# Performance work log

Hardware: AMD Instinct MI355X
Metric: run time of the kernel (lower is better)

## Reference

```python
import jax, jax.numpy as jnp
import numpy as np

N = 100000   # nodes
E = 1600000  # edges
D = 64       # in/hidden channels


def setup_inputs() -> dict:
    key = jax.random.key(0)
    ks = jax.random.split(key, 8)
    x = jax.random.normal(ks[0], (N, D), dtype=jnp.float32)
    edge_index = jax.random.randint(ks[1], (2, E), 0, N, dtype=jnp.int32)
    s = 1.0 / np.sqrt(D)
    W1 = jax.random.uniform(ks[2], (D, D), jnp.float32, -s, s)
    W2 = jax.random.uniform(ks[3], (D, D), jnp.float32, -s, s)
    W3 = jax.random.uniform(ks[4], (D, D), jnp.float32, -s, s)
    b1 = jnp.zeros((D,), jnp.float32)
    b2 = jnp.zeros((D,), jnp.float32)
    b3 = jnp.zeros((D,), jnp.float32)
    return {"x": x, "edge_index": edge_index,
            "W1": W1, "b1": b1, "W2": W2, "b2": b2, "W3": W3, "b3": b3}


def _gcn_conv(x, src, dst, deg_inv_sqrt, W, b):
    # norm = d^{-1/2}[src] * d^{-1/2}[dst] (symmetric GCN normalization w/ self-loops)
    norm = deg_inv_sqrt[src] * deg_inv_sqrt[dst]        # [E+N]
    h = x @ W                                           # [N, D] dense GEMM
    msg = h[src] * norm[:, None]                        # gather + scale
    out = jax.ops.segment_sum(msg, dst, num_segments=x.shape[0])  # scatter-add
    return out + b


def reference(x, edge_index, W1, b1, W2, b2, W3, b3):
    n = x.shape[0]
    loop = jnp.arange(n, dtype=edge_index.dtype)
    src = jnp.concatenate([edge_index[0], loop])        # add self-loops
    dst = jnp.concatenate([edge_index[1], loop])
    deg = jax.ops.segment_sum(jnp.ones_like(src, x.dtype), dst, num_segments=n)
    deg_inv_sqrt = jnp.where(deg > 0, jax.lax.rsqrt(jnp.maximum(deg, 1.0)), 0.0)

    h = _gcn_conv(x, src, dst, deg_inv_sqrt, W1, b1)
    h = jax.nn.relu(h)                                  # dropout is identity (eval)
    h = _gcn_conv(h, src, dst, deg_inv_sqrt, W2, b2)
    h = jax.nn.relu(h)
    out = _gcn_conv(h, src, dst, deg_inv_sqrt, W3, b3)
    return out
```

## Files before the change

### kernel.cpp

```cpp
#include <hip/hip_runtime.h>
#include <hip/hip_fp16.h>
#include <type_traits>

#define DCH 64
#define NBSHIFT 8
#define BROWS 256
#define MAXNB 512
#define CAPB 5120
#define CAP 8192
#define CHUNK 4096
#define SCT 512

__global__ __launch_bounds__(SCT) void bucket_scatter(const int* __restrict__ src,
        const int* __restrict__ dst, int* __restrict__ cursor,
        unsigned int* __restrict__ tmp, int E, int NB) {
    __shared__ int hist[MAXNB];
    __shared__ int loff[MAXNB];
    __shared__ int res[MAXNB];
    __shared__ unsigned int stage[CHUNK];
    __shared__ unsigned short stgb[CHUNK];
    const int base_e = blockIdx.x * CHUNK;
    const int nloc = min(CHUNK, E - base_e);
    const int t = threadIdx.x;
    if (t < NB) hist[t] = 0;
    __syncthreads();
    unsigned int pk[CHUNK / SCT];
    int bk[CHUNK / SCT], rk[CHUNK / SCT];
    #pragma unroll
    for (int c = 0; c < CHUNK / SCT; ++c) {
        int i = t + c * SCT;
        if (i < nloc) {
            int d = dst[base_e + i];
            int b = d >> NBSHIFT;
            rk[c] = atomicAdd(&hist[b], 1);
            bk[c] = b;
            pk[c] = ((unsigned int)(d & (BROWS - 1)) << 24) |
                    (unsigned int)src[base_e + i];
        }
    }
    __syncthreads();
    int v = (t < NB) ? hist[t] : 0;
    loff[t] = v;
    __syncthreads();
    for (int o = 1; o < MAXNB; o <<= 1) {
        int add = (t >= o) ? loff[t - o] : 0;
        __syncthreads();
        loff[t] += add;
        __syncthreads();
    }
    int excl = loff[t] - v;
    loff[t] = excl;
    if (t < NB) res[t] = v ? (t * CAPB + atomicAdd(&cursor[t], v)) : 0;
    __syncthreads();
    #pragma unroll
    for (int c = 0; c < CHUNK / SCT; ++c) {
        int i = t + c * SCT;
        if (i < nloc) {
            int p = loff[bk[c]] + rk[c];
            stage[p] = pk[c];
            stgb[p]  = (unsigned short)bk[c];
        }
    }
    __syncthreads();
    for (int i = t; i < nloc; i += SCT) {
        int b = stgb[i];
        tmp[res[b] + (i - loff[b])] = stage[i];
    }
}

__global__ __launch_bounds__(BROWS) void bucket_to_csr(
        const unsigned int* __restrict__ tmp, const int* __restrict__ cursor,
        int2* __restrict__ range, int* __restrict__ srcs,
        float* __restrict__ dinv, int N) {
    __shared__ int hist[BROWS];
    __shared__ int off[BROWS];
    __shared__ int cur[BROWS];
    __shared__ int stage[CAP];
    const int b = blockIdx.x;
    const int base = b * CAPB;
    const int count = cursor[b];
    const int t = threadIdx.x;
    hist[t] = 0;
    __syncthreads();
    for (int i = t; i < count; i += BROWS)
        atomicAdd(&hist[tmp[base + i] >> 24], 1);
    __syncthreads();
    int v = hist[t];
    off[t] = v;
    __syncthreads();
    for (int o = 1; o < BROWS; o <<= 1) {
        int add = (t >= o) ? off[t - o] : 0;
        __syncthreads();
        off[t] += add;
        __syncthreads();
    }
    int excl = off[t] - v;
    cur[t] = excl;
    int node = (b << NBSHIFT) + t;
    if (node < N) {
        range[node] = make_int2(base + excl, base + excl + v);
        dinv[node]  = rsqrtf((float)v + 1.0f);
    }
    __syncthreads();
    const bool st = (count <= CAP);
    for (int i = t; i < count; i += BROWS) {
        unsigned int p = tmp[base + i];
        int low = p >> 24;
        int s = (int)(p & 0xFFFFFFu);
        int pos = atomicAdd(&cur[low], 1);
        if (st) stage[pos] = s;
        else    srcs[base + pos] = s;
    }
    __syncthreads();
    if (st)
        for (int i = t; i < count; i += BROWS) srcs[base + i] = stage[i];
}

template<typename InT>
__global__ __launch_bounds__(256, 4) void gemm64(const InT* __restrict__ A,
        const float* __restrict__ W, const float* __restrict__ dinv,
        __half* __restrict__ H, int nrows) {
    __shared__ float Wl[64 * 64];
    __shared__ float Al[64 * 68];
    #pragma unroll
    for (int j = 0; j < 4; ++j) {
        int idx = (int)threadIdx.x + j * 256;
        float4 w = ((const float4*)W)[idx];
        *(float4*)&Wl[(idx >> 4) * 64 + (idx & 15) * 4] = w;
    }
    const int tx = threadIdx.x & 15;
    const int ty = threadIdx.x >> 4;
    const int c0 = tx * 4, r0 = ty * 4;
    const int ntiles = (nrows + 63) >> 6;
    for (int tile = blockIdx.x; tile < ntiles; tile += gridDim.x) {
        const int rowbase = tile << 6;
        const int rmax = min(64, nrows - rowbase);
        __syncthreads();
        #pragma unroll
        for (int j = 0; j < 4; ++j) {
            int idx = (int)threadIdx.x + j * 256;
            int r = idx >> 4, kq = idx & 15;
            float4 a;
            if (r < rmax) {
                if constexpr (std::is_same<InT, float>::value) {
                    a = *(const float4*)(A + (size_t)(rowbase + r) * 64 + kq * 4);
                } else {
                    unsigned long long u = *(const unsigned long long*)
                        ((const __half*)A + (size_t)(rowbase + r) * 64 + kq * 4);
                    union { unsigned long long u; __half2 h[2]; } cv; cv.u = u;
                    float2 f0 = __half22float2(cv.h[0]);
                    float2 f1 = __half22float2(cv.h[1]);
                    a = make_float4(f0.x, f0.y, f1.x, f1.y);
                }
            } else a = make_float4(0.f, 0.f, 0.f, 0.f);
            *(float4*)&Al[r * 68 + kq * 4] = a;
        }
        __syncthreads();
        float acc[4][4] = {};
        #pragma unroll 8
        for (int k = 0; k < 64; ++k) {
            float4 wv = *(const float4*)&Wl[k * 64 + c0];
            float a0 = Al[(r0 + 0) * 68 + k];
            float a1 = Al[(r0 + 1) * 68 + k];
            float a2 = Al[(r0 + 2) * 68 + k];
            float a3 = Al[(r0 + 3) * 68 + k];
            acc[0][0] += a0 * wv.x; acc[0][1] += a0 * wv.y; acc[0][2] += a0 * wv.z; acc[0][3] += a0 * wv.w;
            acc[1][0] += a1 * wv.x; acc[1][1] += a1 * wv.y; acc[1][2] += a1 * wv.z; acc[1][3] += a1 * wv.w;
            acc[2][0] += a2 * wv.x; acc[2][1] += a2 * wv.y; acc[2][2] += a2 * wv.z; acc[2][3] += a2 * wv.w;
            acc[3][0] += a3 * wv.x; acc[3][1] += a3 * wv.y; acc[3][2] += a3 * wv.z; acc[3][3] += a3 * wv.w;
        }
        #pragma unroll
        for (int i = 0; i < 4; ++i) {
            int r = r0 + i;
            if (r < rmax) {
                float s = dinv[rowbase + r];
                __half2* ph = (__half2*)(H + (size_t)(rowbase + r) * 64 + c0);
                ph[0] = __floats2half2_rn(acc[i][0] * s, acc[i][1] * s);
                ph[1] = __floats2half2_rn(acc[i][2] * s, acc[i][3] * s);
            }
        }
    }
}

__device__ __forceinline__ void accumh(__half2 acc[4], float4 v) {
    const __half2* hp = (const __half2*)&v;
    #pragma unroll
    for (int j = 0; j < 4; ++j) acc[j] = __hadd2(acc[j], hp[j]);
}

__device__ __forceinline__ float4 row16(const __half* __restrict__ hs, int s, int q) {
    return *(const float4*)((const char*)hs + ((size_t)s << 7) + (q << 4));
}

template<typename OutT>
__global__ __launch_bounds__(256) void aggregate(
    const __half* __restrict__ hs, const int2* __restrict__ range,
    const int* __restrict__ srcs, const float* __restrict__ dinv,
    const float* __restrict__ b, OutT* __restrict__ out, int n, int do_relu)
{
    int wid  = (blockIdx.x * blockDim.x + threadIdx.x) >> 6;
    int lane = threadIdx.x & 63;
    if (wid >= n) return;
    const int g = lane >> 3;
    const int q = lane & 7;
    const int2 be = range[wid];
    const int beg = be.x, end = be.y;
    __half2 zero = __float2half2_rn(0.f);
    __half2 acch[4]  = {zero, zero, zero, zero};
    __half2 acch2[4] = {zero, zero, zero, zero};
    if (g == 7) accumh(acch, row16(hs, wid, q));
    int e = beg + g;
    for (; e + 8 < end; e += 16) {
        int s0 = srcs[e];
        int s1 = srcs[e + 8];
        float4 v0 = row16(hs, s0, q);
        float4 v1 = row16(hs, s1, q);
        accumh(acch, v0);
        accumh(acch2, v1);
    }
    if (e < end) accumh(acch, row16(hs, srcs[e], q));
    float acc[8];
    #pragma unroll
    for (int j = 0; j < 4; ++j) {
        float2 f0 = __half22float2(acch[j]);
        float2 f1 = __half22float2(acch2[j]);
        acc[2 * j]     = f0.x + f1.x;
        acc[2 * j + 1] = f0.y + f1.y;
    }
    #pragma unroll
    for (int j = 0; j < 8; ++j) {
        float a = acc[j];
        a += __shfl_xor(a, 8);
        a += __shfl_xor(a, 16);
        a += __shfl_xor(a, 32);
        acc[j] = a;
    }
    if (g == 0) {
        float dd = dinv[wid];
        float o[8];
        #pragma unroll
        for (int j = 0; j < 8; ++j) {
            float v = acc[j] * dd + b[q * 8 + j];
            o[j] = do_relu ? fmaxf(v, 0.f) : v;
        }
        if constexpr (std::is_same<OutT, __half>::value) {
            union { uint4 u; __half2 h[4]; } cv;
            cv.h[0] = __floats2half2_rn(o[0], o[1]);
            cv.h[1] = __floats2half2_rn(o[2], o[3]);
            cv.h[2] = __floats2half2_rn(o[4], o[5]);
            cv.h[3] = __floats2half2_rn(o[6], o[7]);
            *(uint4*)((__half*)out + (size_t)wid * DCH + q * 8) = cv.u;
        } else {
            float4* po = (float4*)((float*)out + (size_t)wid * DCH + q * 8);
            po[0] = make_float4(o[0], o[1], o[2], o[3]);
            po[1] = make_float4(o[4], o[5], o[6], o[7]);
        }
    }
}

extern "C" void kernel_launch(void* const* d_in, const int* in_sizes, int n_in,
                              void* d_out, int out_size, void* d_ws, size_t ws_size,
                              hipStream_t stream) {
    const float* x  = (const float*)d_in[0];
    const int*   ei = (const int*)d_in[1];
    const float* W1 = (const float*)d_in[2];
    const float* b1 = (const float*)d_in[3];
    const float* W2 = (const float*)d_in[4];
    const float* b2 = (const float*)d_in[5];
    const float* W3 = (const float*)d_in[6];
    const float* b3 = (const float*)d_in[7];

    const int N = in_sizes[0] / DCH;
    const int E = in_sizes[1] / 2;
    const int* src = ei;
    const int* dst = ei + E;
    const int NB = (N + BROWS - 1) >> NBSHIFT;

    char* ws = (char*)d_ws;
    size_t off = 0;
    auto alloc = [&](size_t bytes) { void* p = ws + off; off = (off + bytes + 255) & ~(size_t)255; return p; };
    int*    cursor = (int*)   alloc((size_t)MAXNB * 4);
    int2*   range  = (int2*)  alloc((size_t)N * 8);
    int*    srcs   = (int*)   alloc((size_t)NB * CAPB * 4);
    float*  dinv   = (float*) alloc((size_t)N * 4);
    __half* hs     = (__half*)alloc((size_t)N * DCH * 2);
    __half* agg    = (__half*)alloc((size_t)N * DCH * 2);
    unsigned int* tmp = (unsigned int*)hs;
    float* out = (float*)d_out;

    const int T = 256;
    const int gAG  = (N * DCH + T - 1) / T;
    const int gGM  = (N + 63) / 64;
    const int nchk = (E + CHUNK - 1) / CHUNK;

    hipMemsetAsync(cursor, 0, (size_t)NB * 4, stream);
    bucket_scatter<<<nchk, SCT, 0, stream>>>(src, dst, cursor, tmp, E, NB);
    bucket_to_csr<<<NB, BROWS, 0, stream>>>(tmp, cursor, range, srcs, dinv, N);

    gemm64<float><<<gGM, T, 0, stream>>>(x, W1, dinv, hs, N);
    aggregate<__half><<<gAG, T, 0, stream>>>(hs, range, srcs, dinv, b1, agg, N, 1);

    gemm64<__half><<<gGM, T, 0, stream>>>(agg, W2, dinv, hs, N);
    aggregate<__half><<<gAG, T, 0, stream>>>(hs, range, srcs, dinv, b2, agg, N, 1);

    gemm64<__half><<<gGM, T, 0, stream>>>(agg, W3, dinv, hs, N);
    aggregate<float><<<gAG, T, 0, stream>>>(hs, range, srcs, dinv, b3, out, N, 0);
}
```

Baseline: 223.6 us.

## Replace FP32 SIMT GEMM with FP16 MFMA 16x16x32 matrix-core kernel

Swaps the scalar FP32 register-tiled 64x64 GEMM for a kernel that stages A and a transposed W in LDS as fp16 and computes each 64-row tile with mfma_f32_16x16x32_f16, one wave per 16 rows. The first layer's fp32 input is also converted to fp16, which lowers precision. The goal is to cut GEMM compute time in each of the three layers. In exchange, every block re-converts and transposes W and the output stores are scalar 2-byte writes, which are less coalesced than before.

```diff
diff --git a/kernel.cpp b/kernel.cpp
--- a/kernel.cpp
+++ b/kernel.cpp
@@ -10,6 +10,9 @@
 #define CAP 8192
 #define CHUNK 4096
 #define SCT 512
+
+typedef _Float16 v8h __attribute__((ext_vector_type(8)));
+typedef float    v4f __attribute__((ext_vector_type(4)));
 
 __global__ __launch_bounds__(SCT) void bucket_scatter(const int* __restrict__ src,
         const int* __restrict__ dst, int* __restrict__ cursor,
@@ -117,67 +120,62 @@
 }
 
 template<typename InT>
-__global__ __launch_bounds__(256, 4) void gemm64(const InT* __restrict__ A,
+__global__ __launch_bounds__(256, 4) void gemm_mfma(const InT* __restrict__ A,
         const float* __restrict__ W, const float* __restrict__ dinv,
         __half* __restrict__ H, int nrows) {
-    __shared__ float Wl[64 * 64];
-    __shared__ float Al[64 * 68];
-    #pragma unroll
-    for (int j = 0; j < 4; ++j) {
-        int idx = (int)threadIdx.x + j * 256;
-        float4 w = ((const float4*)W)[idx];
-        *(float4*)&Wl[(idx >> 4) * 64 + (idx & 15) * 4] = w;
-    }
-    const int tx = threadIdx.x & 15;
-    const int ty = threadIdx.x >> 4;
-    const int c0 = tx * 4, r0 = ty * 4;
-    const int ntiles = (nrows + 63) >> 6;
-    for (int tile = blockIdx.x; tile < ntiles; tile += gridDim.x) {
-        const int rowbase = tile << 6;
-        const int rmax = min(64, nrows - rowbase);
-        __syncthreads();
+    __shared__ _Float16 Wt[64 * 72];
+    __shared__ _Float16 Ah[64 * 72];
+    const int t = threadIdx.x;
+    for (int i = t; i < 4096; i += 256) {
+        int k = i >> 6, c = i & 63;
+        Wt[c * 72 + k] = (_Float16)W[i];
+    }
+    const int rowbase = blockIdx.x << 6;
+    const int rmax = min(64, nrows - rowbase);
+    if constexpr (std::is_same<InT, float>::value) {
         #pragma unroll
         for (int j = 0; j < 4; ++j) {
-            int idx = (int)threadIdx.x + j * 256;
-            int r = idx >> 4, kq = idx & 15;
-            float4 a;
-            if (r < rmax) {
-                if constexpr (std::is_same<InT, float>::value) {
-                    a = *(const float4*)(A + (size_t)(rowbase + r) * 64 + kq * 4);
-                } else {
-                    unsigned long long u = *(const unsigned long long*)
-                        ((const __half*)A + (size_t)(rowbase + r) * 64 + kq * 4);
-                    union { unsigned long long u; __half2 h[2]; } cv; cv.u = u;
-                    float2 f0 = __half22float2(cv.h[0]);
-                    float2 f1 = __half22float2(cv.h[1]);
-                    a = make_float4(f0.x, f0.y, f1.x, f1.y);
-                }
-            } else a = make_float4(0.f, 0.f, 0.f, 0.f);
-            *(float4*)&Al[r * 68 + kq * 4] = a;
-        }
-        __syncthreads();
-        float acc[4][4] = {};
-        #pragma unroll 8
-        for (int k = 0; k < 64; ++k) {
-            float4 wv = *(const float4*)&Wl[k * 64 + c0];
-            float a0 = Al[(r0 + 0) * 68 + k];
-            float a1 = Al[(r0 + 1) * 68 + k];
-            float a2 = Al[(r0 + 2) * 68 + k];
-            float a3 = Al[(r0 + 3) * 68 + k];
-            acc[0][0] += a0 * wv.x; acc[0][1] += a0 * wv.y; acc[0][2] += a0 * wv.z; acc[0][3] += a0 * wv.w;
-            acc[1][0] += a1 * wv.x; acc[1][1] += a1 * wv.y; acc[1][2] += a1 * wv.z; acc[1][3] += a1 * wv.w;
-            acc[2][0] += a2 * wv.x; acc[2][1] += a2 * wv.y; acc[2][2] += a2 * wv.z; acc[2][3] += a2 * wv.w;
-            acc[3][0] += a3 * wv.x; acc[3][1] += a3 * wv.y; acc[3][2] += a3 * wv.z; acc[3][3] += a3 * wv.w;
-        }
+            int idx = t + j * 256;
+            int r = idx >> 4, q4 = idx & 15;
+            float4 a = (r < rmax) ? *(const float4*)(A + (size_t)(rowbase + r) * 64 + q4 * 4)
+                                  : make_float4(0.f, 0.f, 0.f, 0.f);
+            union { uint2 u; _Float16 h[4]; } cv;
+            cv.h[0] = (_Float16)a.x; cv.h[1] = (_Float16)a.y;
+            cv.h[2] = (_Float16)a.z; cv.h[3] = (_Float16)a.w;
+            *(uint2*)&Ah[r * 72 + q4 * 4] = cv.u;
+        }
+    } else {
         #pragma unroll
-        for (int i = 0; i < 4; ++i) {
-            int r = r0 + i;
-            if (r < rmax) {
-                float s = dinv[rowbase + r];
-                __half2* ph = (__half2*)(H + (size_t)(rowbase + r) * 64 + c0);
-                ph[0] = __floats2half2_rn(acc[i][0] * s, acc[i][1] * s);
-                ph[1] = __floats2half2_rn(acc[i][2] * s, acc[i][3] * s);
-            }
+        for (int j = 0; j < 2; ++j) {
+            int idx = t + j * 256;
+            int r = idx >> 3, q = idx & 7;
+            uint4 u = (r < rmax) ? *(const uint4*)((const __half*)A + (size_t)(rowbase + r) * 64 + q * 8)
+                                 : make_uint4(0u, 0u, 0u, 0u);
+            *(uint4*)&Ah[r * 72 + q * 8] = u;
+        }
+    }
+    __syncthreads();
+    const int w = t >> 6, lane = t & 63;
+    const int m = lane & 15, kq = lane >> 4;
+    const _Float16* ap = &Ah[(w * 16 + m) * 72 + kq * 8];
+    v4f acc[4] = {{0.f,0.f,0.f,0.f},{0.f,0.f,0.f,0.f},{0.f,0.f,0.f,0.f},{0.f,0.f,0.f,0.f}};
+    #pragma unroll
+    for (int ks = 0; ks < 2; ++ks) {
+        v8h a = *(const v8h*)(ap + ks * 32);
+        #pragma unroll
+        for (int tc = 0; tc < 4; ++tc) {
+            v8h b = *(const v8h*)&Wt[(tc * 16 + m) * 72 + ks * 32 + kq * 8];
+            acc[tc] = __builtin_amdgcn_mfma_f32_16x16x32_f16(a, b, acc[tc], 0, 0, 0);
+        }
+    }
+    #pragma unroll
+    for (int j = 0; j < 4; ++j) {
+        int r = w * 16 + kq * 4 + j;
+        if (r < rmax) {
+            float s = dinv[rowbase + r];
+            #pragma unroll
+            for (int tc = 0; tc < 4; ++tc)
+                H[(size_t)(rowbase + r) * 64 + tc * 16 + m] = __float2half(acc[tc][j] * s);
         }
     }
 }
@@ -297,12 +295,12 @@
     bucket_scatter<<<nchk, SCT, 0, stream>>>(src, dst, cursor, tmp, E, NB);
     bucket_to_csr<<<NB, BROWS, 0, stream>>>(tmp, cursor, range, srcs, dinv, N);
 
-    gemm64<float><<<gGM, T, 0, stream>>>(x, W1, dinv, hs, N);
+    gemm_mfma<float><<<gGM, T, 0, stream>>>(x, W1, dinv, hs, N);
     aggregate<__half><<<gAG, T, 0, stream>>>(hs, range, srcs, dinv, b1, agg, N, 1);
 
-    gemm64<__half><<<gGM, T, 0, stream>>>(agg, W2, dinv, hs, N);
+    gemm_mfma<__half><<<gGM, T, 0, stream>>>(agg, W2, dinv, hs, N);
     aggregate<__half><<<gAG, T, 0, stream>>>(hs, range, srcs, dinv, b2, agg, N, 1);
 
-    gemm64<__half><<<gGM, T, 0, stream>>>(agg, W3, dinv, hs, N);
+    gemm_mfma<__half><<<gGM, T, 0, stream>>>(agg, W3, dinv, hs, N);
     aggregate<float><<<gAG, T, 0, stream>>>(hs, range, srcs, dinv, b3, out, N, 0);
 }
```

Result: faster. 202.6 us (-9.4%).
